# Optimization experiments

Measured on AMD Instinct MI355X. Metric: run time of the kernel, lower is better.

Reference implementation:

```python
import jax, jax.numpy as jnp
import numpy as np

N_NODES = 50000
N_EDGES = 600000
D = 128  # in_channels == out_channels
LN_EPS = 1e-5


def _mlp(h, W1, b1, W2, b2, ln_g, ln_b):
    # anemoi MLP: Linear -> SiLU -> Linear -> LayerNorm
    h = jax.nn.silu(h @ W1 + b1)
    h = h @ W2 + b2
    mu = jnp.mean(h, axis=-1, keepdims=True)
    var = jnp.var(h, axis=-1, keepdims=True)
    return (h - mu) * jax.lax.rsqrt(var + LN_EPS) * ln_g + ln_b


def setup_inputs() -> dict:
    key = jax.random.key(0)
    ks = jax.random.split(key, 12)
    s = lambda fan_in: 1.0 / np.sqrt(fan_in)
    inp = {
        "x": jax.random.normal(ks[0], (N_NODES, D), dtype=jnp.float32),
        "edge_attr": jax.random.normal(ks[1], (N_EDGES, D), dtype=jnp.float32),
        "edge_index": jax.random.randint(ks[2], (2, N_EDGES), 0, N_NODES, dtype=jnp.int32),
        # conv edge-MLP params: in = 3*D (x_dst, x_src, edge_attr)
        "eW1": jax.random.uniform(ks[3], (3 * D, D), jnp.float32, -s(3 * D), s(3 * D)),
        "eb1": jnp.zeros((D,), jnp.float32),
        "eW2": jax.random.uniform(ks[4], (D, D), jnp.float32, -s(D), s(D)),
        "eb2": jnp.zeros((D,), jnp.float32),
        "eln_g": jnp.ones((D,), jnp.float32),
        "eln_b": jnp.zeros((D,), jnp.float32),
        # node MLP params: in = 2*D (x, aggregated messages)
        "nW1": jax.random.uniform(ks[5], (2 * D, D), jnp.float32, -s(2 * D), s(2 * D)),
        "nb1": jnp.zeros((D,), jnp.float32),
        "nW2": jax.random.uniform(ks[6], (D, D), jnp.float32, -s(D), s(D)),
        "nb2": jnp.zeros((D,), jnp.float32),
        "nln_g": jnp.ones((D,), jnp.float32),
        "nln_b": jnp.zeros((D,), jnp.float32),
    }
    return inp


def reference(x, edge_attr, edge_index,
              eW1, eb1, eW2, eb2, eln_g, eln_b,
              nW1, nb1, nW2, nb2, nln_g, nln_b):
    src = edge_index[0]  # j
    dst = edge_index[1]  # i
    # GraphConv.message: edge MLP over cat([x_i, x_j, edge_attr])
    edge_in = jnp.concatenate([x[dst], x[src], edge_attr], axis=1)  # [E, 3D]
    edges_new = _mlp(edge_in, eW1, eb1, eW2, eb2, eln_g, eln_b)      # [E, D]
    # aggregate: scatter-add to destination nodes (chunking sums to the same result)
    out = jax.ops.segment_sum(edges_new, dst, num_segments=x.shape[0])  # [N, D]
    # node update: concat + MLP + residual
    nodes_new = _mlp(jnp.concatenate([x, out], axis=1), nW1, nb1, nW2, nb2, nln_g, nln_b) + x
    return nodes_new, edges_new
```

## Files before the change

kernel.cpp:

```cpp
#include <hip/hip_runtime.h>
#include <hip/hip_bf16.h>

#define D       128
#define NNODES  50000
#define NEDGES  600000
#define TE      64
#define TN      64
#define BLK     256
#define LN_EPS  1e-5f

typedef float  fx4    __attribute__((ext_vector_type(4)));
typedef float  f32x4  __attribute__((ext_vector_type(4)));
typedef __bf16 bf16x4 __attribute__((ext_vector_type(4)));
typedef __bf16 bf16x8 __attribute__((ext_vector_type(8)));

#define EW1F_OFF 0
#define EW2F_OFF (128 * 384)
#define NW1F_OFF (EW2F_OFF + 128 * 128)
#define NW2F_OFF (NW1F_OFF + 128 * 256)
#define WS_ELEMS (NW2F_OFF + 128 * 128)
#define W_BYTES  (WS_ELEMS * 2)
#define AGGB_OFF ((size_t)W_BYTES)
#define WS_NEED  (AGGB_OFF + (size_t)NNODES * D * 2)

__device__ __forceinline__ float silu_f(float z) {
    return z * (1.0f / (1.0f + __expf(-z)));
}

__global__ __launch_bounds__(256) void prep_weights(
    const float* __restrict__ eW1, const float* __restrict__ eW2,
    const float* __restrict__ nW1, const float* __restrict__ nW2,
    __bf16* __restrict__ ws)
{
    int idx = blockIdx.x * 256 + threadIdx.x;
    if (idx >= WS_ELEMS) return;
    const float* src;
    int local;
    if (idx < EW2F_OFF)      { src = eW1; local = idx; }
    else if (idx < NW1F_OFF) { src = eW2; local = idx - EW2F_OFF; }
    else if (idx < NW2F_OFF) { src = nW1; local = idx - NW1F_OFF; }
    else                     { src = nW2; local = idx - NW2F_OFF; }
    const int f   = local >> 9;
    const int rem = local & 511;
    const int l   = rem >> 3;
    const int j   = rem & 7;
    const int ks  = f >> 3;
    const int nf  = f & 7;
    const int n   = (nf << 4) + (l & 15);
    const int k   = (ks << 5) + ((l >> 4) << 3) + j;
    ws[idx] = (__bf16)src[(size_t)k * D + n];
}

template<bool PK>
__global__ __launch_bounds__(BLK, 4) void edge_kernel(
    const float* __restrict__ x,
    const float* __restrict__ edge_attr,
    const int*   __restrict__ edge_index,
    const __bf16* __restrict__ W1f,
    const float* __restrict__ b1,
    const __bf16* __restrict__ W2f,
    const float* __restrict__ b2,
    const float* __restrict__ lng, const float* __restrict__ lnb,
    float* __restrict__ edges_out,
    float* __restrict__ aggF,
    __hip_bfloat162* __restrict__ aggB)
{
    __shared__ __bf16 in_t[TE][264];
    __shared__ int    src_s[TE], dst_s[TE];

    const int tid = threadIdx.x;
    const int e0g = blockIdx.x * TE;

    if (tid < TE) {
        src_s[tid] = edge_index[e0g + tid];
        dst_s[tid] = edge_index[NEDGES + e0g + tid];
    }
    __syncthreads();

    const int lane  = tid & 63;
    const int wid   = tid >> 6;
    const int wrow0 = wid << 4;
    const int c16   = lane & 15;
    const int kq    = lane >> 4;
    const int ks8   = kq << 3;
    const int lo8   = lane << 3;

    bf16x8 aE[4];
    {
        const float* ep = edge_attr + (size_t)(e0g + wrow0 + c16) * D + ks8;
        #pragma unroll
        for (int ks2 = 0; ks2 < 4; ++ks2) {
            fx4 v0 = *(const fx4*)(ep + (ks2 << 5));
            fx4 v1 = *(const fx4*)(ep + (ks2 << 5) + 4);
            bf16x8 a;
            #pragma unroll
            for (int j = 0; j < 4; ++j) { a[j] = (__bf16)v0[j]; a[j + 4] = (__bf16)v1[j]; }
            aE[ks2] = a;
        }
    }

    #pragma unroll
    for (int it = 0; it < 8; ++it) {
        const int idx = tid + it * BLK;
        const int e   = idx >> 5;
        const int c4  = (idx & 31) << 2;
        fx4 v = *(const fx4*)&x[(size_t)dst_s[e] * D + c4];
        bf16x4 h;
        #pragma unroll
        for (int j = 0; j < 4; ++j) h[j] = (__bf16)v[j];
        *(bf16x4*)&in_t[e][c4] = h;
    }
    #pragma unroll
    for (int it = 0; it < 8; ++it) {
        const int idx = tid + it * BLK;
        const int e   = idx >> 5;
        const int c4  = (idx & 31) << 2;
        fx4 v = *(const fx4*)&x[(size_t)src_s[e] * D + c4];
        bf16x4 h;
        #pragma unroll
        for (int j = 0; j < 4; ++j) h[j] = (__bf16)v[j];
        *(bf16x4*)&in_t[e][128 + c4] = h;
    }
    __syncthreads();

    f32x4 acc[8];
    #pragma unroll
    for (int nf = 0; nf < 8; ++nf) acc[nf] = (f32x4){0.f, 0.f, 0.f, 0.f};

    #pragma unroll
    for (int ks = 0; ks < 12; ++ks) {
        bf16x8 a = (ks < 8) ? *(const bf16x8*)&in_t[wrow0 + c16][(ks << 5) + ks8]
                            : aE[ks - 8];
        const __bf16* wp = W1f + ((size_t)(ks << 3) << 9) + lo8;
        #pragma unroll
        for (int nf = 0; nf < 8; ++nf) {
            bf16x8 b = *(const bf16x8*)(wp + (nf << 9));
            acc[nf] = __builtin_amdgcn_mfma_f32_16x16x32_bf16(a, b, acc[nf], 0, 0, 0);
        }
    }

    #pragma unroll
    for (int nf = 0; nf < 8; ++nf) {
        const float bb = b1[nf * 16 + c16];
        #pragma unroll
        for (int r = 0; r < 4; ++r) {
            float h = silu_f(acc[nf][r] + bb);
            in_t[wrow0 + kq * 4 + r][nf * 16 + c16] = (__bf16)h;
        }
    }

    f32x4 acc2[8];
    #pragma unroll
    for (int nf = 0; nf < 8; ++nf) acc2[nf] = (f32x4){0.f, 0.f, 0.f, 0.f};

    #pragma unroll
    for (int ks = 0; ks < 4; ++ks) {
        bf16x8 a = *(const bf16x8*)&in_t[wrow0 + c16][(ks << 5) + ks8];
        const __bf16* wp = W2f + ((size_t)(ks << 3) << 9) + lo8;
        #pragma unroll
        for (int nf = 0; nf < 8; ++nf) {
            bf16x8 b = *(const bf16x8*)(wp + (nf << 9));
            acc2[nf] = __builtin_amdgcn_mfma_f32_16x16x32_bf16(a, b, acc2[nf], 0, 0, 0);
        }
    }

    float b2v[8], gv[8], bvv[8];
    #pragma unroll
    for (int nf = 0; nf < 8; ++nf) {
        b2v[nf] = b2[nf * 16 + c16];
        gv[nf]  = lng[nf * 16 + c16];
        bvv[nf] = lnb[nf * 16 + c16];
    }

    float s[4] = {0.f, 0.f, 0.f, 0.f}, q[4] = {0.f, 0.f, 0.f, 0.f};
    #pragma unroll
    for (int nf = 0; nf < 8; ++nf)
        #pragma unroll
        for (int r = 0; r < 4; ++r) {
            float zz = acc2[nf][r] + b2v[nf];
            acc2[nf][r] = zz;
            s[r] += zz;
            q[r] += zz * zz;
        }
    #pragma unroll
    for (int m = 1; m <= 8; m <<= 1)
        #pragma unroll
        for (int r = 0; r < 4; ++r) {
            s[r] += __shfl_xor(s[r], m, 64);
            q[r] += __shfl_xor(q[r], m, 64);
        }

    #pragma unroll
    for (int r = 0; r < 4; ++r) {
        const float mu   = s[r] * (1.0f / 128.0f);
        const float var  = q[r] * (1.0f / 128.0f) - mu * mu;
        const float rstd = rsqrtf(var + LN_EPS);
        const int row = wrow0 + kq * 4 + r;
        const size_t erow = (size_t)(e0g + row) * D;
        const int dn = dst_s[row];
        #pragma unroll
        for (int nf = 0; nf < 8; ++nf) {
            const int col = nf * 16 + c16;
            float o = (acc2[nf][r] - mu) * rstd * gv[nf] + bvv[nf];
            edges_out[erow + col] = o;
            if constexpr (PK) {
                float on = __shfl_xor(o, 1, 64);
                if ((c16 & 1) == 0) {
                    __hip_bfloat162 v;
                    v.x = __float2bfloat16(o);
                    v.y = __float2bfloat16(on);
                    unsafeAtomicAdd(&aggB[((size_t)dn * D + col) >> 1], v);
                }
            } else {
                atomicAdd(aggF + (size_t)dn * D + col, o);
            }
        }
    }
}

template<bool BF16AGG>
__global__ __launch_bounds__(BLK, 4) void node_kernel(
    const float* __restrict__ x,
    const float* __restrict__ aggF,
    const __bf16* __restrict__ aggB,
    const __bf16* __restrict__ W1f,
    const float* __restrict__ b1,
    const __bf16* __restrict__ W2f,
    const float* __restrict__ b2,
    const float* __restrict__ lng, const float* __restrict__ lnb,
    float* __restrict__ nodes_out)
{
    __shared__ __bf16 in_t[TN][264];

    const int tid = threadIdx.x;
    const int r0g = blockIdx.x * TN;

    #pragma unroll
    for (int it = 0; it < 8; ++it) {
        const int idx = tid + it * BLK;
        const int e   = idx >> 5;
        const int c4  = (idx & 31) << 2;
        const int row = r0g + e;
        fx4 v = {0.f, 0.f, 0.f, 0.f};
        if (row < NNODES) v = *(const fx4*)&x[(size_t)row * D + c4];
        bf16x4 h;
        #pragma unroll
        for (int j = 0; j < 4; ++j) h[j] = (__bf16)v[j];
        *(bf16x4*)&in_t[e][c4] = h;
    }
    #pragma unroll
    for (int it = 0; it < 8; ++it) {
        const int idx = tid + it * BLK;
        const int e   = idx >> 5;
        const int c4  = (idx & 31) << 2;
        const int row = r0g + e;
        bf16x4 h = {(__bf16)0.f, (__bf16)0.f, (__bf16)0.f, (__bf16)0.f};
        if (row < NNODES) {
            if constexpr (BF16AGG) {
                h = *(const bf16x4*)&aggB[(size_t)row * D + c4];
            } else {
                fx4 v = *(const fx4*)&aggF[(size_t)row * D + c4];
                #pragma unroll
                for (int j = 0; j < 4; ++j) h[j] = (__bf16)v[j];
            }
        }
        *(bf16x4*)&in_t[e][128 + c4] = h;
    }
    __syncthreads();

    const int lane  = tid & 63;
    const int wid   = tid >> 6;
    const int wrow0 = wid << 4;
    const int c16   = lane & 15;
    const int kq    = lane >> 4;
    const int ks8   = kq << 3;
    const int lo8   = lane << 3;

    f32x4 acc[8];
    #pragma unroll
    for (int nf = 0; nf < 8; ++nf) acc[nf] = (f32x4){0.f, 0.f, 0.f, 0.f};

    #pragma unroll
    for (int ks = 0; ks < 8; ++ks) {
        bf16x8 a = *(const bf16x8*)&in_t[wrow0 + c16][(ks << 5) + ks8];
        const __bf16* wp = W1f + ((size_t)(ks << 3) << 9) + lo8;
        #pragma unroll
        for (int nf = 0; nf < 8; ++nf) {
            bf16x8 b = *(const bf16x8*)(wp + (nf << 9));
            acc[nf] = __builtin_amdgcn_mfma_f32_16x16x32_bf16(a, b, acc[nf], 0, 0, 0);
        }
    }

    #pragma unroll
    for (int nf = 0; nf < 8; ++nf) {
        const float bb = b1[nf * 16 + c16];
        #pragma unroll
        for (int r = 0; r < 4; ++r) {
            float h = silu_f(acc[nf][r] + bb);
            in_t[wrow0 + kq * 4 + r][nf * 16 + c16] = (__bf16)h;
        }
    }

    f32x4 acc2[8];
    #pragma unroll
    for (int nf = 0; nf < 8; ++nf) acc2[nf] = (f32x4){0.f, 0.f, 0.f, 0.f};

    #pragma unroll
    for (int ks = 0; ks < 4; ++ks) {
        bf16x8 a = *(const bf16x8*)&in_t[wrow0 + c16][(ks << 5) + ks8];
        const __bf16* wp = W2f + ((size_t)(ks << 3) << 9) + lo8;
        #pragma unroll
        for (int nf = 0; nf < 8; ++nf) {
            bf16x8 b = *(const bf16x8*)(wp + (nf << 9));
            acc2[nf] = __builtin_amdgcn_mfma_f32_16x16x32_bf16(a, b, acc2[nf], 0, 0, 0);
        }
    }

    float b2v[8], gv[8], bvv[8];
    #pragma unroll
    for (int nf = 0; nf < 8; ++nf) {
        b2v[nf] = b2[nf * 16 + c16];
        gv[nf]  = lng[nf * 16 + c16];
        bvv[nf] = lnb[nf * 16 + c16];
    }

    float s[4] = {0.f, 0.f, 0.f, 0.f}, q[4] = {0.f, 0.f, 0.f, 0.f};
    #pragma unroll
    for (int nf = 0; nf < 8; ++nf)
        #pragma unroll
        for (int r = 0; r < 4; ++r) {
            float zz = acc2[nf][r] + b2v[nf];
            acc2[nf][r] = zz;
            s[r] += zz;
            q[r] += zz * zz;
        }
    #pragma unroll
    for (int m = 1; m <= 8; m <<= 1)
        #pragma unroll
        for (int r = 0; r < 4; ++r) {
            s[r] += __shfl_xor(s[r], m, 64);
            q[r] += __shfl_xor(q[r], m, 64);
        }

    #pragma unroll
    for (int r = 0; r < 4; ++r) {
        const float mu   = s[r] * (1.0f / 128.0f);
        const float var  = q[r] * (1.0f / 128.0f) - mu * mu;
        const float rstd = rsqrtf(var + LN_EPS);
        const int row = r0g + wrow0 + kq * 4 + r;
        if (row >= NNODES) continue;
        const size_t orow = (size_t)row * D;
        #pragma unroll
        for (int nf = 0; nf < 8; ++nf) {
            const int col = nf * 16 + c16;
            float o = (acc2[nf][r] - mu) * rstd * gv[nf] + bvv[nf] + x[orow + col];
            nodes_out[orow + col] = o;
        }
    }
}

extern "C" void kernel_launch(void* const* d_in, const int* in_sizes, int n_in,
                              void* d_out, int out_size, void* d_ws, size_t ws_size,
                              hipStream_t stream) {
    (void)in_sizes; (void)n_in; (void)out_size;

    const float* x         = (const float*)d_in[0];
    const float* edge_attr = (const float*)d_in[1];
    const int*   edge_idx  = (const int*)  d_in[2];
    const float* eW1 = (const float*)d_in[3];
    const float* eb1 = (const float*)d_in[4];
    const float* eW2 = (const float*)d_in[5];
    const float* eb2 = (const float*)d_in[6];
    const float* elg = (const float*)d_in[7];
    const float* elb = (const float*)d_in[8];
    const float* nW1 = (const float*)d_in[9];
    const float* nb1 = (const float*)d_in[10];
    const float* nW2 = (const float*)d_in[11];
    const float* nb2 = (const float*)d_in[12];
    const float* nlg = (const float*)d_in[13];
    const float* nlb = (const float*)d_in[14];

    float* out       = (float*)d_out;
    float* nodes_out = out;
    float* edges_out = out + (size_t)NNODES * D;

    char*   wsb = (char*)d_ws;
    __bf16* ws  = (__bf16*)d_ws;

    prep_weights<<<(WS_ELEMS + 255) / 256, 256, 0, stream>>>(eW1, eW2, nW1, nW2, ws);

    if (ws_size >= WS_NEED) {
        __bf16* aggB = (__bf16*)(wsb + AGGB_OFF);
        hipMemsetAsync(aggB, 0, (size_t)NNODES * D * 2, stream);

        edge_kernel<true><<<NEDGES / TE, BLK, 0, stream>>>(
            x, edge_attr, edge_idx,
            ws + EW1F_OFF, eb1, ws + EW2F_OFF, eb2, elg, elb,
            edges_out, nullptr, (__hip_bfloat162*)aggB);

        node_kernel<true><<<(NNODES + TN - 1) / TN, BLK, 0, stream>>>(
            x, nullptr, aggB,
            ws + NW1F_OFF, nb1, ws + NW2F_OFF, nb2, nlg, nlb,
            nodes_out);
    } else {
        hipMemsetAsync(nodes_out, 0, (size_t)NNODES * D * sizeof(float), stream);

        edge_kernel<false><<<NEDGES / TE, BLK, 0, stream>>>(
            x, edge_attr, edge_idx,
            ws + EW1F_OFF, eb1, ws + EW2F_OFF, eb2, elg, elb,
            edges_out, nodes_out, nullptr);

        node_kernel<false><<<(NNODES + TN - 1) / TN, BLK, 0, stream>>>(
            x, nodes_out, nullptr,
            ws + NW1F_OFF, nb1, ws + NW2F_OFF, nb2, nlg, nlb,
            nodes_out);
    }
}
```

Baseline: 450.8 us.

## Pre-convert node features to bf16 and gather per-wave without block barriers

Adds a prep kernel that converts x to bf16 once into workspace, so the edge kernel gathers half as many bytes per x_dst/x_src row (16-byte bf16x8 loads instead of fp32 loads plus conversion). The gather is also reorganised so each wave loads only its own 16 rows of indices and features, which removes the two block-wide __syncthreads. This costs an extra kernel launch and a full pass over x, plus more workspace. The fp32 fallback path keeps the same per-wave layout.

Result: slower. 486.8 us (+8.0%).

```diff
diff --git a/kernel.cpp b/kernel.cpp
--- a/kernel.cpp
+++ b/kernel.cpp
@@ -21,7 +21,8 @@
 #define WS_ELEMS (NW2F_OFF + 128 * 128)
 #define W_BYTES  (WS_ELEMS * 2)
 #define AGGB_OFF ((size_t)W_BYTES)
-#define WS_NEED  (AGGB_OFF + (size_t)NNODES * D * 2)
+#define XB_OFF   (AGGB_OFF + (size_t)NNODES * D * 2)
+#define WS_NEED  (XB_OFF   + (size_t)NNODES * D * 2)
 
 __device__ __forceinline__ float silu_f(float z) {
     return z * (1.0f / (1.0f + __expf(-z)));
@@ -51,9 +52,22 @@
     ws[idx] = (__bf16)src[(size_t)k * D + n];
 }
 
-template<bool PK>
+__global__ __launch_bounds__(256) void prep_x(
+    const float* __restrict__ x, __bf16* __restrict__ xB)
+{
+    int idx = blockIdx.x * 256 + threadIdx.x;
+    if (idx >= NNODES * D / 4) return;
+    fx4 v = ((const fx4*)x)[idx];
+    bf16x4 h;
+    #pragma unroll
+    for (int j = 0; j < 4; ++j) h[j] = (__bf16)v[j];
+    ((bf16x4*)xB)[idx] = h;
+}
+
+template<bool PRE>
 __global__ __launch_bounds__(BLK, 4) void edge_kernel(
     const float* __restrict__ x,
+    const __bf16* __restrict__ xB,
     const float* __restrict__ edge_attr,
     const int*   __restrict__ edge_index,
     const __bf16* __restrict__ W1f,
@@ -71,12 +85,6 @@
     const int tid = threadIdx.x;
     const int e0g = blockIdx.x * TE;
 
-    if (tid < TE) {
-        src_s[tid] = edge_index[e0g + tid];
-        dst_s[tid] = edge_index[NEDGES + e0g + tid];
-    }
-    __syncthreads();
-
     const int lane  = tid & 63;
     const int wid   = tid >> 6;
     const int wrow0 = wid << 4;
@@ -85,6 +93,11 @@
     const int ks8   = kq << 3;
     const int lo8   = lane << 3;
 
+    if (lane < 16) {
+        src_s[wrow0 + lane] = edge_index[e0g + wrow0 + lane];
+        dst_s[wrow0 + lane] = edge_index[NEDGES + e0g + wrow0 + lane];
+    }
+
     bf16x8 aE[4];
     {
         const float* ep = edge_attr + (size_t)(e0g + wrow0 + c16) * D + ks8;
@@ -99,29 +112,43 @@
         }
     }
 
-    #pragma unroll
-    for (int it = 0; it < 8; ++it) {
-        const int idx = tid + it * BLK;
-        const int e   = idx >> 5;
-        const int c4  = (idx & 31) << 2;
-        fx4 v = *(const fx4*)&x[(size_t)dst_s[e] * D + c4];
-        bf16x4 h;
-        #pragma unroll
-        for (int j = 0; j < 4; ++j) h[j] = (__bf16)v[j];
-        *(bf16x4*)&in_t[e][c4] = h;
-    }
-    #pragma unroll
-    for (int it = 0; it < 8; ++it) {
-        const int idx = tid + it * BLK;
-        const int e   = idx >> 5;
-        const int c4  = (idx & 31) << 2;
-        fx4 v = *(const fx4*)&x[(size_t)src_s[e] * D + c4];
-        bf16x4 h;
-        #pragma unroll
-        for (int j = 0; j < 4; ++j) h[j] = (__bf16)v[j];
-        *(bf16x4*)&in_t[e][128 + c4] = h;
-    }
-    __syncthreads();
+    if constexpr (PRE) {
+        #pragma unroll
+        for (int p = 0; p < 4; ++p) {
+            const int row = wrow0 + (p << 2) + (lane >> 4);
+            const int c8  = (lane & 15) << 3;
+            bf16x8 v = *(const bf16x8*)&xB[(size_t)dst_s[row] * D + c8];
+            *(bf16x8*)&in_t[row][c8] = v;
+        }
+        #pragma unroll
+        for (int p = 0; p < 4; ++p) {
+            const int row = wrow0 + (p << 2) + (lane >> 4);
+            const int c8  = (lane & 15) << 3;
+            bf16x8 v = *(const bf16x8*)&xB[(size_t)src_s[row] * D + c8];
+            *(bf16x8*)&in_t[row][128 + c8] = v;
+        }
+    } else {
+        #pragma unroll
+        for (int p = 0; p < 8; ++p) {
+            const int row = wrow0 + (p << 1) + (lane >> 5);
+            const int c4  = (lane & 31) << 2;
+            fx4 v = *(const fx4*)&x[(size_t)dst_s[row] * D + c4];
+            bf16x4 h;
+            #pragma unroll
+            for (int j = 0; j < 4; ++j) h[j] = (__bf16)v[j];
+            *(bf16x4*)&in_t[row][c4] = h;
+        }
+        #pragma unroll
+        for (int p = 0; p < 8; ++p) {
+            const int row = wrow0 + (p << 1) + (lane >> 5);
+            const int c4  = (lane & 31) << 2;
+            fx4 v = *(const fx4*)&x[(size_t)src_s[row] * D + c4];
+            bf16x4 h;
+            #pragma unroll
+            for (int j = 0; j < 4; ++j) h[j] = (__bf16)v[j];
+            *(bf16x4*)&in_t[row][128 + c4] = h;
+        }
+    }
 
     f32x4 acc[8];
     #pragma unroll
@@ -203,7 +230,7 @@
             const int col = nf * 16 + c16;
             float o = (acc2[nf][r] - mu) * rstd * gv[nf] + bvv[nf];
             edges_out[erow + col] = o;
-            if constexpr (PK) {
+            if constexpr (PRE) {
                 float on = __shfl_xor(o, 1, 64);
                 if ((c16 & 1) == 0) {
                     __hip_bfloat162 v;
@@ -391,10 +418,13 @@
 
     if (ws_size >= WS_NEED) {
         __bf16* aggB = (__bf16*)(wsb + AGGB_OFF);
+        __bf16* xB   = (__bf16*)(wsb + XB_OFF);
+
+        prep_x<<<(NNODES * D / 4 + 255) / 256, 256, 0, stream>>>(x, xB);
         hipMemsetAsync(aggB, 0, (size_t)NNODES * D * 2, stream);
 
         edge_kernel<true><<<NEDGES / TE, BLK, 0, stream>>>(
-            x, edge_attr, edge_idx,
+            x, xB, edge_attr, edge_idx,
             ws + EW1F_OFF, eb1, ws + EW2F_OFF, eb2, elg, elb,
             edges_out, nullptr, (__hip_bfloat162*)aggB);
 
@@ -406,7 +436,7 @@
         hipMemsetAsync(nodes_out, 0, (size_t)NNODES * D * sizeof(float), stream);
 
         edge_kernel<false><<<NEDGES / TE, BLK, 0, stream>>>(
-            x, edge_attr, edge_idx,
+            x, nullptr, edge_attr, edge_idx,
             ws + EW1F_OFF, eb1, ws + EW2F_OFF, eb2, elg, elb,
             edges_out, nodes_out, nullptr);
 
```

## Use persistent edge kernel with bf16 node features and prefetched gathers

Applied to the files above, without the earlier changes.

Adds a prep pass that converts x to bf16 once, so each edge gather reads half the bytes. The edge kernel becomes persistent with a fixed grid of 1024 blocks striding over tiles. While the current tile's MLP and atomics run, it prefetches the next tile's indices and gathered x rows into registers. The cost is an extra conversion kernel, added workspace, and higher register pressure from holding the prefetch buffers.

Result: slower. 1.711 ms (+279.4%).

```diff
diff --git a/kernel.cpp b/kernel.cpp
--- a/kernel.cpp
+++ b/kernel.cpp
@@ -4,6 +4,8 @@
 #define D       128
 #define NNODES  50000
 #define NEDGES  600000
+#define NTILES  (NEDGES / 64)
+#define GRID_E  1024
 #define TE      64
 #define TN      64
 #define BLK     256
@@ -21,7 +23,8 @@
 #define WS_ELEMS (NW2F_OFF + 128 * 128)
 #define W_BYTES  (WS_ELEMS * 2)
 #define AGGB_OFF ((size_t)W_BYTES)
-#define WS_NEED  (AGGB_OFF + (size_t)NNODES * D * 2)
+#define XB_OFF   (AGGB_OFF + (size_t)NNODES * D * 2)
+#define WS_NEED  (XB_OFF   + (size_t)NNODES * D * 2)
 
 __device__ __forceinline__ float silu_f(float z) {
     return z * (1.0f / (1.0f + __expf(-z)));
@@ -51,8 +54,204 @@
     ws[idx] = (__bf16)src[(size_t)k * D + n];
 }
 
-template<bool PK>
-__global__ __launch_bounds__(BLK, 4) void edge_kernel(
+__global__ __launch_bounds__(256) void prep_x(
+    const float* __restrict__ x, __bf16* __restrict__ xB)
+{
+    int idx = blockIdx.x * 256 + threadIdx.x;
+    if (idx >= NNODES * D / 4) return;
+    fx4 v = ((const fx4*)x)[idx];
+    bf16x4 h;
+    #pragma unroll
+    for (int j = 0; j < 4; ++j) h[j] = (__bf16)v[j];
+    ((bf16x4*)xB)[idx] = h;
+}
+
+__global__ __launch_bounds__(BLK, 4) void edge_kernel_pipe(
+    const __bf16* __restrict__ xB,
+    const float* __restrict__ edge_attr,
+    const int*   __restrict__ edge_index,
+    const __bf16* __restrict__ W1f,
+    const float* __restrict__ b1,
+    const __bf16* __restrict__ W2f,
+    const float* __restrict__ b2,
+    const float* __restrict__ lng, const float* __restrict__ lnb,
+    float* __restrict__ edges_out,
+    __hip_bfloat162* __restrict__ aggB)
+{
+    __shared__ __bf16 in_t[TE][264];
+
+    const int tid   = threadIdx.x;
+    const int lane  = tid & 63;
+    const int wid   = tid >> 6;
+    const int wrow0 = wid << 4;
+    const int c16   = lane & 15;
+    const int kq    = lane >> 4;
+    const int ks8   = kq << 3;
+    const int lo8   = lane << 3;
+    const int gr    = lane >> 4;
+    const int gc8   = (lane & 15) << 3;
+
+    float b1v[8];
+    float b2v[8], gv[8], bvv[8];
+    #pragma unroll
+    for (int nf = 0; nf < 8; ++nf) {
+        b1v[nf] = b1[nf * 16 + c16];
+        b2v[nf] = b2[nf * 16 + c16];
+        gv[nf]  = lng[nf * 16 + c16];
+        bvv[nf] = lnb[nf * 16 + c16];
+    }
+
+    int t = blockIdx.x;
+
+    int id_s_nxt = 0, id_d_nxt = 0;
+    bf16x8 gb_d[4], gb_s[4];
+    {
+        const int base = (t << 6) + wrow0;
+        if (lane < 16) {
+            id_s_nxt = edge_index[base + lane];
+            id_d_nxt = edge_index[NEDGES + base + lane];
+        }
+        #pragma unroll
+        for (int p = 0; p < 4; ++p) {
+            const int rl = (p << 2) + gr;
+            const int dn = __shfl(id_d_nxt, rl, 64);
+            const int sn = __shfl(id_s_nxt, rl, 64);
+            gb_d[p] = *(const bf16x8*)&xB[(size_t)dn * D + gc8];
+            gb_s[p] = *(const bf16x8*)&xB[(size_t)sn * D + gc8];
+        }
+    }
+
+    while (t < NTILES) {
+        const int e0g = t << 6;
+        const int id_s_cur = id_s_nxt;
+        const int id_d_cur = id_d_nxt;
+        (void)id_s_cur;
+
+        #pragma unroll
+        for (int p = 0; p < 4; ++p) {
+            const int row = wrow0 + (p << 2) + gr;
+            *(bf16x8*)&in_t[row][gc8]       = gb_d[p];
+            *(bf16x8*)&in_t[row][128 + gc8] = gb_s[p];
+        }
+
+        const int tn = t + GRID_E;
+        const int tc = (tn < NTILES) ? tn : t;
+        {
+            const int base = (tc << 6) + wrow0;
+            if (lane < 16) {
+                id_s_nxt = edge_index[base + lane];
+                id_d_nxt = edge_index[NEDGES + base + lane];
+            }
+            #pragma unroll
+            for (int p = 0; p < 4; ++p) {
+                const int rl = (p << 2) + gr;
+                const int dn = __shfl(id_d_nxt, rl, 64);
+                const int sn = __shfl(id_s_nxt, rl, 64);
+                gb_d[p] = *(const bf16x8*)&xB[(size_t)dn * D + gc8];
+                gb_s[p] = *(const bf16x8*)&xB[(size_t)sn * D + gc8];
+            }
+        }
+
+        bf16x8 aE[4];
+        {
+            const float* ep = edge_attr + (size_t)(e0g + wrow0 + c16) * D + ks8;
+            #pragma unroll
+            for (int ks2 = 0; ks2 < 4; ++ks2) {
+                fx4 v0 = *(const fx4*)(ep + (ks2 << 5));
+                fx4 v1 = *(const fx4*)(ep + (ks2 << 5) + 4);
+                bf16x8 a;
+                #pragma unroll
+                for (int j = 0; j < 4; ++j) { a[j] = (__bf16)v0[j]; a[j + 4] = (__bf16)v1[j]; }
+                aE[ks2] = a;
+            }
+        }
+
+        f32x4 acc[8];
+        #pragma unroll
+        for (int nf = 0; nf < 8; ++nf) acc[nf] = (f32x4){0.f, 0.f, 0.f, 0.f};
+
+        #pragma unroll
+        for (int ks = 0; ks < 12; ++ks) {
+            bf16x8 a = (ks < 8) ? *(const bf16x8*)&in_t[wrow0 + c16][(ks << 5) + ks8]
+                                : aE[ks - 8];
+            const __bf16* wp = W1f + ((size_t)(ks << 3) << 9) + lo8;
+            #pragma unroll
+            for (int nf = 0; nf < 8; ++nf) {
+                bf16x8 b = *(const bf16x8*)(wp + (nf << 9));
+                acc[nf] = __builtin_amdgcn_mfma_f32_16x16x32_bf16(a, b, acc[nf], 0, 0, 0);
+            }
+        }
+
+        #pragma unroll
+        for (int nf = 0; nf < 8; ++nf) {
+            #pragma unroll
+            for (int r = 0; r < 4; ++r) {
+                float h = silu_f(acc[nf][r] + b1v[nf]);
+                in_t[wrow0 + kq * 4 + r][nf * 16 + c16] = (__bf16)h;
+            }
+        }
+
+        f32x4 acc2[8];
+        #pragma unroll
+        for (int nf = 0; nf < 8; ++nf) acc2[nf] = (f32x4){0.f, 0.f, 0.f, 0.f};
+
+        #pragma unroll
+        for (int ks = 0; ks < 4; ++ks) {
+            bf16x8 a = *(const bf16x8*)&in_t[wrow0 + c16][(ks << 5) + ks8];
+            const __bf16* wp = W2f + ((size_t)(ks << 3) << 9) + lo8;
+            #pragma unroll
+            for (int nf = 0; nf < 8; ++nf) {
+                bf16x8 b = *(const bf16x8*)(wp + (nf << 9));
+                acc2[nf] = __builtin_amdgcn_mfma_f32_16x16x32_bf16(a, b, acc2[nf], 0, 0, 0);
+            }
+        }
+
+        float s[4] = {0.f, 0.f, 0.f, 0.f}, q[4] = {0.f, 0.f, 0.f, 0.f};
+        #pragma unroll
+        for (int nf = 0; nf < 8; ++nf)
+            #pragma unroll
+            for (int r = 0; r < 4; ++r) {
+                float zz = acc2[nf][r] + b2v[nf];
+                acc2[nf][r] = zz;
+                s[r] += zz;
+                q[r] += zz * zz;
+            }
+        #pragma unroll
+        for (int m = 1; m <= 8; m <<= 1)
+            #pragma unroll
+            for (int r = 0; r < 4; ++r) {
+                s[r] += __shfl_xor(s[r], m, 64);
+                q[r] += __shfl_xor(q[r], m, 64);
+            }
+
+        #pragma unroll
+        for (int r = 0; r < 4; ++r) {
+            const float mu   = s[r] * (1.0f / 128.0f);
+            const float var  = q[r] * (1.0f / 128.0f) - mu * mu;
+            const float rstd = rsqrtf(var + LN_EPS);
+            const int rl  = kq * 4 + r;
+            const int dn  = __shfl(id_d_cur, rl, 64);
+            const size_t erow = (size_t)(e0g + wrow0 + rl) * D;
+            #pragma unroll
+            for (int nf = 0; nf < 8; ++nf) {
+                const int col = nf * 16 + c16;
+                float o = (acc2[nf][r] - mu) * rstd * gv[nf] + bvv[nf];
+                edges_out[erow + col] = o;
+                float on = __shfl_xor(o, 1, 64);
+                if ((c16 & 1) == 0) {
+                    __hip_bfloat162 v;
+                    v.x = __float2bfloat16(o);
+                    v.y = __float2bfloat16(on);
+                    unsafeAtomicAdd(&aggB[((size_t)dn * D + col) >> 1], v);
+                }
+            }
+        }
+
+        t = tn;
+    }
+}
+
+__global__ __launch_bounds__(BLK, 4) void edge_kernel_fb(
     const float* __restrict__ x,
     const float* __restrict__ edge_attr,
     const int*   __restrict__ edge_index,
@@ -62,8 +261,7 @@
     const float* __restrict__ b2,
     const float* __restrict__ lng, const float* __restrict__ lnb,
     float* __restrict__ edges_out,
-    float* __restrict__ aggF,
-    __hip_bfloat162* __restrict__ aggB)
+    float* __restrict__ aggF)
 {
     __shared__ __bf16 in_t[TE][264];
     __shared__ int    src_s[TE], dst_s[TE];
@@ -203,17 +401,7 @@
             const int col = nf * 16 + c16;
             float o = (acc2[nf][r] - mu) * rstd * gv[nf] + bvv[nf];
             edges_out[erow + col] = o;
-            if constexpr (PK) {
-                float on = __shfl_xor(o, 1, 64);
-                if ((c16 & 1) == 0) {
-                    __hip_bfloat162 v;
-                    v.x = __float2bfloat16(o);
-                    v.y = __float2bfloat16(on);
-                    unsafeAtomicAdd(&aggB[((size_t)dn * D + col) >> 1], v);
-                }
-            } else {
-                atomicAdd(aggF + (size_t)dn * D + col, o);
-            }
+            atomicAdd(aggF + (size_t)dn * D + col, o);
         }
     }
 }
@@ -391,12 +579,15 @@
 
     if (ws_size >= WS_NEED) {
         __bf16* aggB = (__bf16*)(wsb + AGGB_OFF);
+        __bf16* xB   = (__bf16*)(wsb + XB_OFF);
+
+        prep_x<<<(NNODES * D / 4 + 255) / 256, 256, 0, stream>>>(x, xB);
         hipMemsetAsync(aggB, 0, (size_t)NNODES * D * 2, stream);
 
-        edge_kernel<true><<<NEDGES / TE, BLK, 0, stream>>>(
-            x, edge_attr, edge_idx,
+        edge_kernel_pipe<<<GRID_E, BLK, 0, stream>>>(
+            xB, edge_attr, edge_idx,
             ws + EW1F_OFF, eb1, ws + EW2F_OFF, eb2, elg, elb,
-            edges_out, nullptr, (__hip_bfloat162*)aggB);
+            edges_out, (__hip_bfloat162*)aggB);
 
         node_kernel<true><<<(NNODES + TN - 1) / TN, BLK, 0, stream>>>(
             x, nullptr, aggB,
@@ -405,10 +596,10 @@
     } else {
         hipMemsetAsync(nodes_out, 0, (size_t)NNODES * D * sizeof(float), stream);
 
-        edge_kernel<false><<<NEDGES / TE, BLK, 0, stream>>>(
+        edge_kernel_fb<<<NEDGES / TE, BLK, 0, stream>>>(
             x, edge_attr, edge_idx,
             ws + EW1F_OFF, eb1, ws + EW2F_OFF, eb2, elg, elb,
-            edges_out, nodes_out, nullptr);
+            edges_out, nodes_out);
 
         node_kernel<false><<<(NNODES + TN - 1) / TN, BLK, 0, stream>>>(
             x, nodes_out, nullptr,
```
